# Kernel tuning notes

Hardware: AMD Instinct MI355X
Metric: run time of the kernel (lower is better)

The kernel has to match this reference:

```python
import jax, jax.numpy as jnp
import numpy as np
from jax import lax

EPS = 1e-12


def _conv_block(x, w, scale, bias, pool):
    # x: (N, Cin, H, W), w: (Cout, Cin, 3, 3). BN in eval mode folded into scale/bias.
    y = lax.conv_general_dilated(x, w, window_strides=(1, 1), padding='SAME',
                                 dimension_numbers=('NCHW', 'OIHW', 'NCHW'))
    y = y * scale[None, :, None, None] + bias[None, :, None, None]
    y = jax.nn.relu(y)
    if pool:
        y = lax.reduce_window(y, -jnp.inf, lax.max, (1, 1, 2, 2), (1, 1, 2, 2), 'VALID')
    return y


def _encoder(x, w1, s1, b1, w2, s2, b2, w3, s3, b3, w4, s4, b4):
    x = _conv_block(x, w1, s1, b1, True)
    x = _conv_block(x, w2, s2, b2, True)
    x = _conv_block(x, w3, s3, b3, False)
    x = _conv_block(x, w4, s4, b4, False)
    return x  # (N, 64, 21, 21)


def _l2norm(x, axis):
    n = jnp.sqrt(jnp.sum(x * x, axis=axis, keepdims=True))
    return x / jnp.maximum(n, EPS)


def setup_inputs() -> dict:
    key = jax.random.key(0)
    ks = jax.random.split(key, 8)
    B, NQ, Way, Shot, C, H, W = 2, 75, 5, 5, 3, 84, 84
    D = 64
    inp = {
        'query': jax.random.normal(ks[0], (B, NQ, C, H, W), jnp.float32),
        'support': jax.random.normal(ks[1], (B, Way, Shot, C, H, W), jnp.float32),
        'w1': jax.random.normal(ks[2], (D, C, 3, 3), jnp.float32) * 0.1,
        'w2': jax.random.normal(ks[3], (D, D, 3, 3), jnp.float32) * 0.05,
        'w3': jax.random.normal(ks[4], (D, D, 3, 3), jnp.float32) * 0.05,
        'w4': jax.random.normal(ks[5], (D, D, 3, 3), jnp.float32) * 0.05,
    }
    for i in range(1, 5):
        inp[f's{i}'] = jnp.ones((D,), jnp.float32)
        inp[f'b{i}'] = jnp.zeros((D,), jnp.float32)
    return inp


def reference(query, support, w1, s1, b1, w2, s2, b2, w3, s3, b3, w4, s4, b4):
    B, NQ, C, H, W = query.shape
    _, Way, Shot, _, _, _ = support.shape
    q_flat = query.reshape(B * NQ, C, H, W)
    s_flat = support.reshape(B * Way * Shot, C, H, W)
    q_feat = _encoder(q_flat, w1, s1, b1, w2, s2, b2, w3, s3, b3, w4, s4, b4)
    s_feat = _encoder(s_flat, w1, s1, b1, w2, s2, b2, w3, s3, b3, w4, s4, b4)
    D, h, w = q_feat.shape[1], q_feat.shape[2], q_feat.shape[3]
    HW = h * w
    q_local = _l2norm(q_feat.reshape(B, NQ, D, HW), axis=2)            # (B,NQ,D,HW)
    s_local = s_feat.reshape(B, Way, Shot, D, HW).mean(axis=2)          # mean over shots
    s_local = _l2norm(s_local, axis=2)                                  # (B,Way,D,HW)
    # all pairwise local cosine similarities, batched in one einsum
    sim = jnp.einsum('bqdm,bcdn->bqcmn', q_local, s_local)              # (B,NQ,Way,HW,HW)
    best = sim.max(axis=-1)                                             # best match per query descriptor
    scores = best.mean(axis=-1)                                         # (B,NQ,Way)
    return scores.reshape(B * NQ, Way)
```

## Files before the change

kernel.cpp:

```cpp
#include <hip/hip_runtime.h>

#define EPS 1e-12f

#define NIMG   200
#define NQIMG  150
#define BDIM   2
#define NQ     75
#define WAY    5
#define SHOT   5
#define DCH    64
#define H1     84
#define H2     42
#define H3     21
#define HW2    1764
#define HW3    441
#define PH     86
#define PSZ    7396
#define SST    448

typedef __attribute__((ext_vector_type(8))) short bf16x8;
typedef __attribute__((ext_vector_type(4))) float f32x4;

__device__ __forceinline__ unsigned short f2bf(float f) {
    unsigned u = __float_as_uint(f);
    u += 0x7fffu + ((u >> 16) & 1u);
    return (unsigned short)(u >> 16);
}
__device__ __forceinline__ float bf2f(unsigned short h) {
    return __uint_as_float(((unsigned)h) << 16);
}
__device__ __forceinline__ int swz(int pix, int c) {
    return pix * 128 + ((c ^ ((pix >> 1) & 7)) << 4);
}

__global__ __launch_bounds__(256) void pad_in(
    const float* __restrict__ qin, const float* __restrict__ sin_,
    unsigned short* __restrict__ pad)
{
    int idx = blockIdx.x * 256 + threadIdx.x;
    if (idx >= NIMG * 3 * PSZ) return;
    int img = idx / (3 * PSZ);
    int rem = idx % (3 * PSZ);
    int ci = rem / PSZ, p = rem % PSZ;
    int iy = p / PH, ix = p % PH;
    float v = 0.f;
    if (iy >= 1 && iy <= H1 && ix >= 1 && ix <= H1) {
        const float* src = (img < NQIMG) ? (qin + (size_t)img * 3 * H1 * H1)
                                         : (sin_ + (size_t)(img - NQIMG) * 3 * H1 * H1);
        v = src[(size_t)ci * H1 * H1 + (iy - 1) * H1 + (ix - 1)];
    }
    pad[idx] = f2bf(v);
}

__global__ __launch_bounds__(256) void pack_w1(
    const float* __restrict__ w1, const float* __restrict__ s1,
    unsigned short* __restrict__ p1)
{
    int idx = blockIdx.x * 256 + threadIdx.x;
    if (idx >= 2048) return;
    int j = idx & 7, lane = (idx >> 3) & 63, mt = idx >> 9;
    int co = (mt << 4) + (lane & 15);
    int k = ((lane >> 4) << 3) + j;
    float v = 0.f;
    if (k < 27) {
        int ci = k / 9, s = k % 9;
        v = w1[(co * 3 + ci) * 9 + s] * s1[co];
    }
    p1[idx] = f2bf(v);
}

__global__ __launch_bounds__(256) void pack_w(
    const float* __restrict__ w2, const float* __restrict__ s2,
    const float* __restrict__ w3, const float* __restrict__ s3,
    const float* __restrict__ w4, const float* __restrict__ s4,
    unsigned short* __restrict__ p2, unsigned short* __restrict__ p3,
    unsigned short* __restrict__ p4)
{
    int idx = blockIdx.x * 256 + threadIdx.x;
    if (idx >= 3 * 36864) return;
    int which = idx / 36864;
    int r = idx % 36864;
    int j = r & 7, lane = (r >> 3) & 63, mt = (r >> 9) & 3, t = (r >> 11) & 1, s = r >> 12;
    int co = (mt << 4) + (lane & 15);
    int ci = (t << 5) + ((lane >> 4) << 3) + j;
    const float* w = (which == 0) ? w2 : (which == 1) ? w3 : w4;
    const float* sc = (which == 0) ? s2 : (which == 1) ? s3 : s4;
    unsigned short* p = (which == 0) ? p2 : (which == 1) ? p3 : p4;
    p[r] = f2bf(w[(co * 64 + ci) * 9 + s] * sc[co]);
}

__global__ __launch_bounds__(256) void conv1_mfma(
    const unsigned short* __restrict__ pad,
    const unsigned short* __restrict__ wp1,
    const float* __restrict__ bias,
    unsigned short* __restrict__ out)
{
    int img = blockIdx.x / 7, seg = blockIdx.x % 7;
    int tid = threadIdx.x;
    __shared__ unsigned short strip[3 * 14 * 86];

    const unsigned* srcd = (const unsigned*)pad;
    size_t ibase = (size_t)img * 3 * (PSZ / 2);
    #pragma unroll
    for (int it = 0; it < 8; it++) {
        int i = it * 256 + tid;
        if (i < 1806) {
            int ci = i / 602, r = i % 602;
            ((unsigned*)strip)[i] = srcd[ibase + ci * (PSZ / 2) + 516 * seg + r];
        }
    }
    __syncthreads();

    int wv = tid >> 6, lane = tid & 63;
    int lc = lane & 15, kg = lane >> 4;

    const bf16x8* wvv = (const bf16x8*)wp1;
    bf16x8 a0 = wvv[lane];
    bf16x8 a1 = wvv[64 + lane];
    bf16x8 a2 = wvv[128 + lane];
    bf16x8 a3 = wvv[192 + lane];

    int off[8];
    #pragma unroll
    for (int j = 0; j < 8; j++) {
        int k = (kg << 3) + j;
        int kk = k < 27 ? k : 0;
        int ci = kk / 9, s = kk % 9;
        off[j] = ci * 1204 + (s / 3) * 86 + (s % 3);
    }

    f32x4 bini[4];
    #pragma unroll
    for (int mt = 0; mt < 4; mt++) {
        float4 bq = *reinterpret_cast<const float4*>(bias + (mt << 4) + (kg << 2));
        bini[mt] = (f32x4){bq.x, bq.y, bq.z, bq.w};
    }

    #pragma unroll
    for (int it = 0; it < 4; it++) {
        int pl = it * 64 + wv * 16 + lc;
        bool valid = pl < 252;
        int plc = valid ? pl : 251;
        int pyl = plc / 42, pxl = plc % 42;
        int base = pyl * 172 + 2 * pxl;

        bf16x8 b[4];
        #pragma unroll
        for (int j = 0; j < 8; j++) {
            int a = base + off[j];
            b[0][j] = (short)strip[a];
            b[1][j] = (short)strip[a + 1];
            b[2][j] = (short)strip[a + 86];
            b[3][j] = (short)strip[a + 87];
        }

        f32x4 acc[4][4];
        #pragma unroll
        for (int mt = 0; mt < 4; mt++)
            #pragma unroll
            for (int sub = 0; sub < 4; sub++)
                acc[mt][sub] = bini[mt];
        #pragma unroll
        for (int sub = 0; sub < 4; sub++) {
            acc[0][sub] = __builtin_amdgcn_mfma_f32_16x16x32_bf16(a0, b[sub], acc[0][sub], 0, 0, 0);
            acc[1][sub] = __builtin_amdgcn_mfma_f32_16x16x32_bf16(a1, b[sub], acc[1][sub], 0, 0, 0);
            acc[2][sub] = __builtin_amdgcn_mfma_f32_16x16x32_bf16(a2, b[sub], acc[2][sub], 0, 0, 0);
            acc[3][sub] = __builtin_amdgcn_mfma_f32_16x16x32_bf16(a3, b[sub], acc[3][sub], 0, 0, 0);
        }

        if (valid) {
            int p = seg * 252 + pl;
            #pragma unroll
            for (int mt = 0; mt < 4; mt++) {
                unsigned short uo[4];
                #pragma unroll
                for (int r = 0; r < 4; r++) {
                    float m = fmaxf(fmaxf(acc[mt][0][r], acc[mt][1][r]),
                                    fmaxf(acc[mt][2][r], acc[mt][3][r]));
                    uo[r] = f2bf(fmaxf(m, 0.f));
                }
                uint2 pk;
                pk.x = (unsigned)uo[0] | ((unsigned)uo[1] << 16);
                pk.y = (unsigned)uo[2] | ((unsigned)uo[3] << 16);
                *reinterpret_cast<uint2*>(out + ((size_t)img * HW2 + p) * DCH + (mt << 4) + (kg << 2)) = pk;
            }
        }
    }
}

__global__ __launch_bounds__(256) void conv2_mfma_pool(
    const unsigned short* __restrict__ act,
    const unsigned short* __restrict__ wp,
    const float* __restrict__ bias,
    unsigned short* __restrict__ out)
{
    int img = blockIdx.x / 7, tg = blockIdx.x % 7;
    int tid = threadIdx.x;
    __shared__ unsigned short lds[8 * 44 * DCH];

    const unsigned short* ab = act + (size_t)img * HW2 * DCH;
    int ybase = 6 * tg - 1;
    #pragma unroll
    for (int it = 0; it < 11; it++) {
        int idx = it * 256 + tid;
        int pix = idx >> 3, c = idx & 7;
        int r = pix / 44, xx = pix % 44;
        int y = ybase + r, x = xx - 1;
        bf16x8 v = (bf16x8)(short)0;
        if ((unsigned)y < (unsigned)H2 && (unsigned)x < (unsigned)H2)
            v = *(const bf16x8*)(ab + ((size_t)(y * H2 + x)) * DCH + (c << 3));
        *(bf16x8*)((char*)lds + swz(pix, c)) = v;
    }
    __syncthreads();

    int wv = tid >> 6, lane = tid & 63;
    int lc = lane & 15, kg = lane >> 4;
    int p_local = wv * 16 + lc;
    bool valid = p_local < 63;
    int pl = valid ? p_local : 62;
    int pyl = pl / 21, pxl = pl % 21;
    int pixc[4];
    #pragma unroll
    for (int sub = 0; sub < 4; sub++)
        pixc[sub] = (2 * pyl + (sub >> 1) + 1) * 44 + (2 * pxl + (sub & 1) + 1);

    f32x4 bini[4];
    #pragma unroll
    for (int mt = 0; mt < 4; mt++) {
        float4 bq = *reinterpret_cast<const float4*>(bias + (mt << 4) + (kg << 2));
        bini[mt] = (f32x4){bq.x, bq.y, bq.z, bq.w};
    }

    const bf16x8* wvv = (const bf16x8*)wp;
    f32x4 acc[4][4];
    #pragma unroll
    for (int i = 0; i < 4; i++)
        #pragma unroll
        for (int j = 0; j < 4; j++)
            acc[i][j] = bini[i];

    for (int s = 0; s < 9; s++) {
        int offs = (s / 3 - 1) * 44 + (s % 3 - 1);
        #pragma unroll
        for (int t = 0; t < 2; t++) {
            int fbase = ((s * 2 + t) * 4) << 6;
            bf16x8 a0 = wvv[fbase + lane];
            bf16x8 a1 = wvv[fbase + 64 + lane];
            bf16x8 a2 = wvv[fbase + 128 + lane];
            bf16x8 a3 = wvv[fbase + 192 + lane];
            int c = (t << 2) + kg;
            bf16x8 b[4];
            #pragma unroll
            for (int sub = 0; sub < 4; sub++) {
                int pix = pixc[sub] + offs;
                b[sub] = *(const bf16x8*)((const char*)lds + swz(pix, c));
            }
            #pragma unroll
            for (int sub = 0; sub < 4; sub++) {
                acc[0][sub] = __builtin_amdgcn_mfma_f32_16x16x32_bf16(a0, b[sub], acc[0][sub], 0, 0, 0);
                acc[1][sub] = __builtin_amdgcn_mfma_f32_16x16x32_bf16(a1, b[sub], acc[1][sub], 0, 0, 0);
                acc[2][sub] = __builtin_amdgcn_mfma_f32_16x16x32_bf16(a2, b[sub], acc[2][sub], 0, 0, 0);
                acc[3][sub] = __builtin_amdgcn_mfma_f32_16x16x32_bf16(a3, b[sub], acc[3][sub], 0, 0, 0);
            }
        }
    }

    if (!valid) return;
    int p = tg * 63 + p_local;
    #pragma unroll
    for (int mt = 0; mt < 4; mt++) {
        unsigned short uo[4];
        #pragma unroll
        for (int r = 0; r < 4; r++) {
            float m = fmaxf(fmaxf(acc[mt][0][r], acc[mt][1][r]),
                            fmaxf(acc[mt][2][r], acc[mt][3][r]));
            uo[r] = f2bf(fmaxf(m, 0.f));
        }
        uint2 pk;
        pk.x = (unsigned)uo[0] | ((unsigned)uo[1] << 16);
        pk.y = (unsigned)uo[2] | ((unsigned)uo[3] << 16);
        *reinterpret_cast<uint2*>(out + ((size_t)img * HW3 + p) * DCH + (mt << 4) + (kg << 2)) = pk;
    }
}

__global__ __launch_bounds__(256) void conv34_mfma(
    const unsigned short* __restrict__ act,
    const unsigned short* __restrict__ wp,
    const float* __restrict__ bias,
    unsigned short* __restrict__ out)
{
    int img = blockIdx.x;
    int tid = threadIdx.x;
    __shared__ unsigned short lds[529 * DCH];

    const unsigned short* ab = act + (size_t)img * HW3 * DCH;
    #pragma unroll
    for (int it = 0; it < 17; it++) {
        int idx = it * 256 + tid;
        if (idx < 529 * 8) {
            int pix = idx >> 3, c = idx & 7;
            int r = pix / 23, xx = pix % 23;
            int y = r - 1, x = xx - 1;
            bf16x8 v = (bf16x8)(short)0;
            if ((unsigned)y < (unsigned)H3 && (unsigned)x < (unsigned)H3)
                v = *(const bf16x8*)(ab + ((size_t)(y * H3 + x)) * DCH + (c << 3));
            *(bf16x8*)((char*)lds + swz(pix, c)) = v;
        }
    }
    __syncthreads();

    int wv = tid >> 6, lane = tid & 63;
    int lc = lane & 15, kg = lane >> 4;
    int pixBase[7];
    bool pv[7];
    #pragma unroll
    for (int i = 0; i < 7; i++) {
        int p = (wv * 7 + i) * 16 + lc;
        pv[i] = p < HW3;
        int pc = pv[i] ? p : HW3 - 1;
        pixBase[i] = (pc / 21) * 23 + (pc % 21);
    }

    f32x4 bini[4];
    #pragma unroll
    for (int mt = 0; mt < 4; mt++) {
        float4 bq = *reinterpret_cast<const float4*>(bias + (mt << 4) + (kg << 2));
        bini[mt] = (f32x4){bq.x, bq.y, bq.z, bq.w};
    }

    const bf16x8* wvv = (const bf16x8*)wp;
    f32x4 acc[7][4];
    #pragma unroll
    for (int i = 0; i < 7; i++)
        #pragma unroll
        for (int m = 0; m < 4; m++)
            acc[i][m] = bini[m];

    for (int s = 0; s < 9; s++) {
        int offs = (s / 3) * 23 + (s % 3);
        #pragma unroll
        for (int t = 0; t < 2; t++) {
            int fbase = ((s * 2 + t) * 4) << 6;
            bf16x8 a0 = wvv[fbase + lane];
            bf16x8 a1 = wvv[fbase + 64 + lane];
            bf16x8 a2 = wvv[fbase + 128 + lane];
            bf16x8 a3 = wvv[fbase + 192 + lane];
            int c = (t << 2) + kg;
            #pragma unroll
            for (int i = 0; i < 7; i++) {
                int pix = pixBase[i] + offs;
                bf16x8 bb = *(const bf16x8*)((const char*)lds + swz(pix, c));
                acc[i][0] = __builtin_amdgcn_mfma_f32_16x16x32_bf16(a0, bb, acc[i][0], 0, 0, 0);
                acc[i][1] = __builtin_amdgcn_mfma_f32_16x16x32_bf16(a1, bb, acc[i][1], 0, 0, 0);
                acc[i][2] = __builtin_amdgcn_mfma_f32_16x16x32_bf16(a2, bb, acc[i][2], 0, 0, 0);
                acc[i][3] = __builtin_amdgcn_mfma_f32_16x16x32_bf16(a3, bb, acc[i][3], 0, 0, 0);
            }
        }
    }

    #pragma unroll
    for (int mt = 0; mt < 4; mt++) {
        #pragma unroll
        for (int i = 0; i < 7; i++) {
            if (!pv[i]) continue;
            int p = (wv * 7 + i) * 16 + lc;
            unsigned short uo[4];
            #pragma unroll
            for (int r = 0; r < 4; r++)
                uo[r] = f2bf(fmaxf(acc[i][mt][r], 0.f));
            uint2 pk;
            pk.x = (unsigned)uo[0] | ((unsigned)uo[1] << 16);
            pk.y = (unsigned)uo[2] | ((unsigned)uo[3] << 16);
            *reinterpret_cast<uint2*>(out + ((size_t)img * HW3 + p) * DCH + (mt << 4) + (kg << 2)) = pk;
        }
    }
}

__global__ __launch_bounds__(256) void q_norm(
    const unsigned short* __restrict__ feat, unsigned short* __restrict__ q_local)
{
    int idx = blockIdx.x * 256 + threadIdx.x;
    if (idx >= NQIMG * HW3) return;
    const bf16x8* f = (const bf16x8*)(feat + (size_t)idx * DCH);
    float v[DCH];
    float ss = 0.f;
    #pragma unroll
    for (int g = 0; g < 8; g++) {
        bf16x8 x = f[g];
        #pragma unroll
        for (int j = 0; j < 8; j++) {
            float vv = bf2f((unsigned short)x[j]);
            v[g * 8 + j] = vv;
            ss = fmaf(vv, vv, ss);
        }
    }
    float inv = 1.f / fmaxf(sqrtf(ss), EPS);
    bf16x8* o = (bf16x8*)(q_local + (size_t)idx * DCH);
    #pragma unroll
    for (int g = 0; g < 8; g++) {
        bf16x8 pk;
        #pragma unroll
        for (int j = 0; j < 8; j++) pk[j] = (short)f2bf(v[g * 8 + j] * inv);
        o[g] = pk;
    }
}

__global__ __launch_bounds__(256) void s_mean_norm(
    const unsigned short* __restrict__ feat, unsigned short* __restrict__ s_local)
{
    int idx = blockIdx.x * 256 + threadIdx.x;
    if (idx >= BDIM * WAY * SST) return;
    int hw = idx % SST;
    int bc = idx / SST;
    bf16x8* o = (bf16x8*)(s_local + (size_t)idx * DCH);
    if (hw >= HW3) {
        #pragma unroll
        for (int g = 0; g < 8; g++) o[g] = (bf16x8)(short)0;
        return;
    }
    int img0 = NQIMG + bc * SHOT;
    float v[DCH];
    #pragma unroll
    for (int d = 0; d < DCH; d++) v[d] = 0.f;
    for (int sh = 0; sh < SHOT; sh++) {
        const bf16x8* f = (const bf16x8*)(feat + ((size_t)(img0 + sh) * HW3 + hw) * DCH);
        #pragma unroll
        for (int g = 0; g < 8; g++) {
            bf16x8 x = f[g];
            #pragma unroll
            for (int j = 0; j < 8; j++)
                v[g * 8 + j] += bf2f((unsigned short)x[j]);
        }
    }
    float ss = 0.f;
    #pragma unroll
    for (int d = 0; d < DCH; d++) {
        v[d] *= (1.f / SHOT);
        ss = fmaf(v[d], v[d], ss);
    }
    float inv = 1.f / fmaxf(sqrtf(ss), EPS);
    #pragma unroll
    for (int g = 0; g < 8; g++) {
        bf16x8 pk;
        #pragma unroll
        for (int j = 0; j < 8; j++) pk[j] = (short)f2bf(v[g * 8 + j] * inv);
        o[g] = pk;
    }
}

__global__ __launch_bounds__(256) void sim_mfma(
    const unsigned short* __restrict__ qloc,
    const unsigned short* __restrict__ sloc,
    float* __restrict__ out)
{
    int blk = blockIdx.x;
    int imgq = blk / WAY, way = blk % WAY;
    int b = imgq / NQ;
    const unsigned short* qp = qloc + (size_t)imgq * HW3 * DCH;
    const unsigned short* sp = sloc + (size_t)(b * WAY + way) * SST * DCH;

    int tid = threadIdx.x;
    int wv = tid >> 6, lane = tid & 63;
    int lc = lane & 15, kg = lane >> 4;
    int mt0 = wv * 7;

    bf16x8 qa0[7], qa1[7];
    #pragma unroll
    for (int i = 0; i < 7; i++) {
        const unsigned short* qrow = qp + (size_t)((mt0 + i) * 16 + lc) * DCH + (kg << 3);
        qa0[i] = *(const bf16x8*)(qrow);
        qa1[i] = *(const bf16x8*)(qrow + 32);
    }
    f32x4 rmax[7];
    #pragma unroll
    for (int i = 0; i < 7; i++)
        rmax[i] = (f32x4){-1e30f, -1e30f, -1e30f, -1e30f};

    const f32x4 z4 = (f32x4){0.f, 0.f, 0.f, 0.f};
    const unsigned short* sbase = sp + (size_t)lc * DCH + (kg << 3);

    for (int t = 0; t < 13; t++) {
        const unsigned short* r0 = sbase + (size_t)(2 * t) * 16 * DCH;
        const unsigned short* r1 = r0 + 16 * DCH;
        bf16x8 sA0 = *(const bf16x8*)(r0);
        bf16x8 sA1 = *(const bf16x8*)(r0 + 32);
        bf16x8 sB0 = *(const bf16x8*)(r1);
        bf16x8 sB1 = *(const bf16x8*)(r1 + 32);
        #pragma unroll
        for (int i = 0; i < 7; i++) {
            f32x4 aA = __builtin_amdgcn_mfma_f32_16x16x32_bf16(qa0[i], sA0, z4, 0, 0, 0);
            aA = __builtin_amdgcn_mfma_f32_16x16x32_bf16(qa1[i], sA1, aA, 0, 0, 0);
            f32x4 aB = __builtin_amdgcn_mfma_f32_16x16x32_bf16(qa0[i], sB0, z4, 0, 0, 0);
            aB = __builtin_amdgcn_mfma_f32_16x16x32_bf16(qa1[i], sB1, aB, 0, 0, 0);
            #pragma unroll
            for (int r = 0; r < 4; r++)
                rmax[i][r] = fmaxf(rmax[i][r], fmaxf(aA[r], aB[r]));
        }
    }
    {
        const unsigned short* r0 = sbase + (size_t)26 * 16 * DCH;
        const unsigned short* r1 = r0 + 16 * DCH;
        bf16x8 sA0 = *(const bf16x8*)(r0);
        bf16x8 sA1 = *(const bf16x8*)(r0 + 32);
        bf16x8 sB0 = *(const bf16x8*)(r1);
        bf16x8 sB1 = *(const bf16x8*)(r1 + 32);
        bool nval = (432 + lc) < HW3;
        #pragma unroll
        for (int i = 0; i < 7; i++) {
            f32x4 aA = __builtin_amdgcn_mfma_f32_16x16x32_bf16(qa0[i], sA0, z4, 0, 0, 0);
            aA = __builtin_amdgcn_mfma_f32_16x16x32_bf16(qa1[i], sA1, aA, 0, 0, 0);
            f32x4 aB = __builtin_amdgcn_mfma_f32_16x16x32_bf16(qa0[i], sB0, z4, 0, 0, 0);
            aB = __builtin_amdgcn_mfma_f32_16x16x32_bf16(qa1[i], sB1, aB, 0, 0, 0);
            #pragma unroll
            for (int r = 0; r < 4; r++)
                rmax[i][r] = fmaxf(rmax[i][r], fmaxf(aA[r], nval ? aB[r] : -1e30f));
        }
    }

    float msum = 0.f;
    #pragma unroll
    for (int i = 0; i < 7; i++) {
        #pragma unroll
        for (int r = 0; r < 4; r++) {
            float v = rmax[i][r];
            v = fmaxf(v, __shfl_xor(v, 1, 64));
            v = fmaxf(v, __shfl_xor(v, 2, 64));
            v = fmaxf(v, __shfl_xor(v, 4, 64));
            v = fmaxf(v, __shfl_xor(v, 8, 64));
            int m = (mt0 + i) * 16 + (kg << 2) + r;
            if (lc == 0 && m < HW3) msum += v;
        }
    }
    #pragma unroll
    for (int off = 32; off > 0; off >>= 1)
        msum += __shfl_xor(msum, off, 64);
    __shared__ float red[4];
    if (lane == 0) red[wv] = msum;
    __syncthreads();
    if (tid == 0)
        out[(size_t)imgq * WAY + way] = (red[0] + red[1] + red[2] + red[3]) * (1.f / HW3);
}

extern "C" void kernel_launch(void* const* d_in, const int* in_sizes, int n_in,
                              void* d_out, int out_size, void* d_ws, size_t ws_size,
                              hipStream_t stream) {
    const float* query   = (const float*)d_in[0];
    const float* support = (const float*)d_in[1];
    const float* w1 = (const float*)d_in[2];
    const float* w2 = (const float*)d_in[3];
    const float* w3 = (const float*)d_in[4];
    const float* w4 = (const float*)d_in[5];
    const float* s1 = (const float*)d_in[6];
    const float* b1 = (const float*)d_in[7];
    const float* s2 = (const float*)d_in[8];
    const float* b2 = (const float*)d_in[9];
    const float* s3 = (const float*)d_in[10];
    const float* b3 = (const float*)d_in[11];
    const float* s4 = (const float*)d_in[12];
    const float* b4 = (const float*)d_in[13];
    float* out = (float*)d_out;

    char* ws = (char*)d_ws;
    unsigned short* A1  = (unsigned short*)(ws);
    unsigned short* A2  = (unsigned short*)(ws + 45158400);
    unsigned short* A3  = (unsigned short*)(ws + 56448000);
    unsigned short* A4  = (unsigned short*)(ws + 67737600);
    unsigned short* QL  = (unsigned short*)(ws + 79027200);
    unsigned short* SL  = (unsigned short*)(ws + 87494400);
    unsigned short* WP2 = (unsigned short*)(ws + 88067840);
    unsigned short* WP3 = (unsigned short*)(ws + 88141568);
    unsigned short* WP4 = (unsigned short*)(ws + 88215296);
    unsigned short* WP1 = (unsigned short*)(ws + 88289024);
    unsigned short* PAD = (unsigned short*)(ws + 88293120);

    pad_in<<<(NIMG * 3 * PSZ + 255) / 256, 256, 0, stream>>>(query, support, PAD);
    pack_w1<<<8, 256, 0, stream>>>(w1, s1, WP1);
    pack_w<<<(3 * 36864 + 255) / 256, 256, 0, stream>>>(w2, s2, w3, s3, w4, s4, WP2, WP3, WP4);

    conv1_mfma<<<NIMG * 7, 256, 0, stream>>>(PAD, WP1, b1, A1);
    conv2_mfma_pool<<<NIMG * 7, 256, 0, stream>>>(A1, WP2, b2, A2);
    conv34_mfma<<<NIMG, 256, 0, stream>>>(A2, WP3, b3, A3);
    conv34_mfma<<<NIMG, 256, 0, stream>>>(A3, WP4, b4, A4);

    q_norm<<<(NQIMG * HW3 + 255) / 256, 256, 0, stream>>>(A4, QL);
    s_mean_norm<<<(BDIM * WAY * SST + 255) / 256, 256, 0, stream>>>(A4, SL);

    sim_mfma<<<NQIMG * WAY, 256, 0, stream>>>(QL, SL, out);
}
```

Before: 153.6 us.

## Fuse conv3, conv4 and query L2-norm into one kernel; merge prep kernels

Merges the padding and weight-packing kernels into a single launch. Conv3 and conv4 now run in one kernel: conv3 output is written back into the padded LDS tile, the halo is re-zeroed, and conv4 computes from LDS. For query images the epilogue applies the L2 normalisation in registers via cross-lane shuffles, so the A3 round trip, the separate q_norm pass and several launches are removed. The cost is that each block does twice the work on only 200 blocks, so fewer waves are in flight while the two convolutions run.

```diff
diff --git a/kernel.cpp b/kernel.cpp
--- a/kernel.cpp
+++ b/kernel.cpp
@@ -18,6 +18,10 @@
 #define PSZ    7396
 #define SST    448
 
+#define PAD_BLKS  17335
+#define W1_BLKS   8
+#define W_BLKS    432
+
 typedef __attribute__((ext_vector_type(8))) short bf16x8;
 typedef __attribute__((ext_vector_type(4))) float f32x4;
 
@@ -33,60 +37,54 @@
     return pix * 128 + ((c ^ ((pix >> 1) & 7)) << 4);
 }
 
-__global__ __launch_bounds__(256) void pad_in(
+__global__ __launch_bounds__(256) void prep(
     const float* __restrict__ qin, const float* __restrict__ sin_,
-    unsigned short* __restrict__ pad)
-{
-    int idx = blockIdx.x * 256 + threadIdx.x;
-    if (idx >= NIMG * 3 * PSZ) return;
-    int img = idx / (3 * PSZ);
-    int rem = idx % (3 * PSZ);
-    int ci = rem / PSZ, p = rem % PSZ;
-    int iy = p / PH, ix = p % PH;
-    float v = 0.f;
-    if (iy >= 1 && iy <= H1 && ix >= 1 && ix <= H1) {
-        const float* src = (img < NQIMG) ? (qin + (size_t)img * 3 * H1 * H1)
-                                         : (sin_ + (size_t)(img - NQIMG) * 3 * H1 * H1);
-        v = src[(size_t)ci * H1 * H1 + (iy - 1) * H1 + (ix - 1)];
-    }
-    pad[idx] = f2bf(v);
-}
-
-__global__ __launch_bounds__(256) void pack_w1(
     const float* __restrict__ w1, const float* __restrict__ s1,
-    unsigned short* __restrict__ p1)
-{
-    int idx = blockIdx.x * 256 + threadIdx.x;
-    if (idx >= 2048) return;
-    int j = idx & 7, lane = (idx >> 3) & 63, mt = idx >> 9;
-    int co = (mt << 4) + (lane & 15);
-    int k = ((lane >> 4) << 3) + j;
-    float v = 0.f;
-    if (k < 27) {
-        int ci = k / 9, s = k % 9;
-        v = w1[(co * 3 + ci) * 9 + s] * s1[co];
-    }
-    p1[idx] = f2bf(v);
-}
-
-__global__ __launch_bounds__(256) void pack_w(
     const float* __restrict__ w2, const float* __restrict__ s2,
     const float* __restrict__ w3, const float* __restrict__ s3,
     const float* __restrict__ w4, const float* __restrict__ s4,
+    unsigned short* __restrict__ pad, unsigned short* __restrict__ p1,
     unsigned short* __restrict__ p2, unsigned short* __restrict__ p3,
     unsigned short* __restrict__ p4)
 {
-    int idx = blockIdx.x * 256 + threadIdx.x;
-    if (idx >= 3 * 36864) return;
-    int which = idx / 36864;
-    int r = idx % 36864;
-    int j = r & 7, lane = (r >> 3) & 63, mt = (r >> 9) & 3, t = (r >> 11) & 1, s = r >> 12;
-    int co = (mt << 4) + (lane & 15);
-    int ci = (t << 5) + ((lane >> 4) << 3) + j;
-    const float* w = (which == 0) ? w2 : (which == 1) ? w3 : w4;
-    const float* sc = (which == 0) ? s2 : (which == 1) ? s3 : s4;
-    unsigned short* p = (which == 0) ? p2 : (which == 1) ? p3 : p4;
-    p[r] = f2bf(w[(co * 64 + ci) * 9 + s] * sc[co]);
+    int blk = blockIdx.x;
+    if (blk < PAD_BLKS) {
+        int idx = blk * 256 + threadIdx.x;
+        if (idx >= NIMG * 3 * PSZ) return;
+        int img = idx / (3 * PSZ);
+        int rem = idx % (3 * PSZ);
+        int ci = rem / PSZ, p = rem % PSZ;
+        int iy = p / PH, ix = p % PH;
+        float v = 0.f;
+        if (iy >= 1 && iy <= H1 && ix >= 1 && ix <= H1) {
+            const float* src = (img < NQIMG) ? (qin + (size_t)img * 3 * H1 * H1)
+                                             : (sin_ + (size_t)(img - NQIMG) * 3 * H1 * H1);
+            v = src[(size_t)ci * H1 * H1 + (iy - 1) * H1 + (ix - 1)];
+        }
+        pad[idx] = f2bf(v);
+    } else if (blk < PAD_BLKS + W1_BLKS) {
+        int idx = (blk - PAD_BLKS) * 256 + threadIdx.x;
+        int j = idx & 7, lane = (idx >> 3) & 63, mt = idx >> 9;
+        int co = (mt << 4) + (lane & 15);
+        int k = ((lane >> 4) << 3) + j;
+        float v = 0.f;
+        if (k < 27) {
+            int ci = k / 9, s = k % 9;
+            v = w1[(co * 3 + ci) * 9 + s] * s1[co];
+        }
+        p1[idx] = f2bf(v);
+    } else {
+        int idx = (blk - PAD_BLKS - W1_BLKS) * 256 + threadIdx.x;
+        int which = idx / 36864;
+        int r = idx % 36864;
+        int j = r & 7, lane = (r >> 3) & 63, mt = (r >> 9) & 3, t = (r >> 11) & 1, s = r >> 12;
+        int co = (mt << 4) + (lane & 15);
+        int ci = (t << 5) + ((lane >> 4) << 3) + j;
+        const float* w = (which == 0) ? w2 : (which == 1) ? w3 : w4;
+        const float* sc = (which == 0) ? s2 : (which == 1) ? s3 : s4;
+        unsigned short* p = (which == 0) ? p2 : (which == 1) ? p3 : p4;
+        p[r] = f2bf(w[(co * 64 + ci) * 9 + s] * sc[co]);
+    }
 }
 
 __global__ __launch_bounds__(256) void conv1_mfma(
@@ -283,11 +281,12 @@
     }
 }
 
-__global__ __launch_bounds__(256) void conv34_mfma(
+__global__ __launch_bounds__(256) void conv34_fused(
     const unsigned short* __restrict__ act,
-    const unsigned short* __restrict__ wp,
-    const float* __restrict__ bias,
-    unsigned short* __restrict__ out)
+    const unsigned short* __restrict__ wp3, const unsigned short* __restrict__ wp4,
+    const float* __restrict__ b3, const float* __restrict__ b4,
+    unsigned short* __restrict__ a4out,
+    unsigned short* __restrict__ qlout)
 {
     int img = blockIdx.x;
     int tid = threadIdx.x;
@@ -324,11 +323,10 @@
     f32x4 bini[4];
     #pragma unroll
     for (int mt = 0; mt < 4; mt++) {
-        float4 bq = *reinterpret_cast<const float4*>(bias + (mt << 4) + (kg << 2));
+        float4 bq = *reinterpret_cast<const float4*>(b3 + (mt << 4) + (kg << 2));
         bini[mt] = (f32x4){bq.x, bq.y, bq.z, bq.w};
     }
 
-    const bf16x8* wvv = (const bf16x8*)wp;
     f32x4 acc[7][4];
     #pragma unroll
     for (int i = 0; i < 7; i++)
@@ -336,15 +334,16 @@
         for (int m = 0; m < 4; m++)
             acc[i][m] = bini[m];
 
+    const bf16x8* wv3 = (const bf16x8*)wp3;
     for (int s = 0; s < 9; s++) {
         int offs = (s / 3) * 23 + (s % 3);
         #pragma unroll
         for (int t = 0; t < 2; t++) {
             int fbase = ((s * 2 + t) * 4) << 6;
-            bf16x8 a0 = wvv[fbase + lane];
-            bf16x8 a1 = wvv[fbase + 64 + lane];
-            bf16x8 a2 = wvv[fbase + 128 + lane];
-            bf16x8 a3 = wvv[fbase + 192 + lane];
+            bf16x8 a0 = wv3[fbase + lane];
+            bf16x8 a1 = wv3[fbase + 64 + lane];
+            bf16x8 a2 = wv3[fbase + 128 + lane];
+            bf16x8 a3 = wv3[fbase + 192 + lane];
             int c = (t << 2) + kg;
             #pragma unroll
             for (int i = 0; i < 7; i++) {
@@ -358,12 +357,14 @@
         }
     }
 
-    #pragma unroll
-    for (int mt = 0; mt < 4; mt++) {
-        #pragma unroll
-        for (int i = 0; i < 7; i++) {
-            if (!pv[i]) continue;
-            int p = (wv * 7 + i) * 16 + lc;
+    __syncthreads();
+
+    #pragma unroll
+    for (int i = 0; i < 7; i++) {
+        if (!pv[i]) continue;
+        int pix = pixBase[i] + 24;
+        #pragma unroll
+        for (int mt = 0; mt < 4; mt++) {
             unsigned short uo[4];
             #pragma unroll
             for (int r = 0; r < 4; r++)
@@ -371,37 +372,105 @@
             uint2 pk;
             pk.x = (unsigned)uo[0] | ((unsigned)uo[1] << 16);
             pk.y = (unsigned)uo[2] | ((unsigned)uo[3] << 16);
-            *reinterpret_cast<uint2*>(out + ((size_t)img * HW3 + p) * DCH + (mt << 4) + (kg << 2)) = pk;
-        }
-    }
-}
-
-__global__ __launch_bounds__(256) void q_norm(
-    const unsigned short* __restrict__ feat, unsigned short* __restrict__ q_local)
-{
-    int idx = blockIdx.x * 256 + threadIdx.x;
-    if (idx >= NQIMG * HW3) return;
-    const bf16x8* f = (const bf16x8*)(feat + (size_t)idx * DCH);
-    float v[DCH];
-    float ss = 0.f;
-    #pragma unroll
-    for (int g = 0; g < 8; g++) {
-        bf16x8 x = f[g];
-        #pragma unroll
-        for (int j = 0; j < 8; j++) {
-            float vv = bf2f((unsigned short)x[j]);
-            v[g * 8 + j] = vv;
-            ss = fmaf(vv, vv, ss);
-        }
-    }
-    float inv = 1.f / fmaxf(sqrtf(ss), EPS);
-    bf16x8* o = (bf16x8*)(q_local + (size_t)idx * DCH);
-    #pragma unroll
-    for (int g = 0; g < 8; g++) {
-        bf16x8 pk;
-        #pragma unroll
-        for (int j = 0; j < 8; j++) pk[j] = (short)f2bf(v[g * 8 + j] * inv);
-        o[g] = pk;
+            int c = (mt << 1) + (kg >> 1);
+            *(uint2*)((char*)lds + swz(pix, c) + ((kg & 1) << 3)) = pk;
+        }
+    }
+    #pragma unroll
+    for (int it = 0; it < 3; it++) {
+        int idx = it * 256 + tid;
+        if (idx < 704) {
+            int j = idx >> 3, c = idx & 7;
+            int pix;
+            if (j < 23)      pix = j;
+            else if (j < 46) pix = 506 + (j - 23);
+            else { int k = j - 46; pix = (1 + (k >> 1)) * 23 + (k & 1) * 22; }
+            *(bf16x8*)((char*)lds + swz(pix, c)) = (bf16x8)(short)0;
+        }
+    }
+    __syncthreads();
+
+    #pragma unroll
+    for (int mt = 0; mt < 4; mt++) {
+        float4 bq = *reinterpret_cast<const float4*>(b4 + (mt << 4) + (kg << 2));
+        bini[mt] = (f32x4){bq.x, bq.y, bq.z, bq.w};
+    }
+    #pragma unroll
+    for (int i = 0; i < 7; i++)
+        #pragma unroll
+        for (int m = 0; m < 4; m++)
+            acc[i][m] = bini[m];
+
+    const bf16x8* wv4 = (const bf16x8*)wp4;
+    for (int s = 0; s < 9; s++) {
+        int offs = (s / 3) * 23 + (s % 3);
+        #pragma unroll
+        for (int t = 0; t < 2; t++) {
+            int fbase = ((s * 2 + t) * 4) << 6;
+            bf16x8 a0 = wv4[fbase + lane];
+            bf16x8 a1 = wv4[fbase + 64 + lane];
+            bf16x8 a2 = wv4[fbase + 128 + lane];
+            bf16x8 a3 = wv4[fbase + 192 + lane];
+            int c = (t << 2) + kg;
+            #pragma unroll
+            for (int i = 0; i < 7; i++) {
+                int pix = pixBase[i] + offs;
+                bf16x8 bb = *(const bf16x8*)((const char*)lds + swz(pix, c));
+                acc[i][0] = __builtin_amdgcn_mfma_f32_16x16x32_bf16(a0, bb, acc[i][0], 0, 0, 0);
+                acc[i][1] = __builtin_amdgcn_mfma_f32_16x16x32_bf16(a1, bb, acc[i][1], 0, 0, 0);
+                acc[i][2] = __builtin_amdgcn_mfma_f32_16x16x32_bf16(a2, bb, acc[i][2], 0, 0, 0);
+                acc[i][3] = __builtin_amdgcn_mfma_f32_16x16x32_bf16(a3, bb, acc[i][3], 0, 0, 0);
+            }
+        }
+    }
+
+    if (img < NQIMG) {
+        #pragma unroll
+        for (int i = 0; i < 7; i++) {
+            float v[4][4];
+            float ssq = 0.f;
+            #pragma unroll
+            for (int mt = 0; mt < 4; mt++)
+                #pragma unroll
+                for (int r = 0; r < 4; r++) {
+                    float x = fmaxf(acc[i][mt][r], 0.f);
+                    v[mt][r] = x;
+                    ssq = fmaf(x, x, ssq);
+                }
+            ssq += __shfl_xor(ssq, 16, 64);
+            ssq += __shfl_xor(ssq, 32, 64);
+            float inv = 1.f / fmaxf(sqrtf(ssq), EPS);
+            if (!pv[i]) continue;
+            int p = (wv * 7 + i) * 16 + lc;
+            #pragma unroll
+            for (int mt = 0; mt < 4; mt++) {
+                unsigned short uo[4];
+                #pragma unroll
+                for (int r = 0; r < 4; r++)
+                    uo[r] = f2bf(v[mt][r] * inv);
+                uint2 pk;
+                pk.x = (unsigned)uo[0] | ((unsigned)uo[1] << 16);
+                pk.y = (unsigned)uo[2] | ((unsigned)uo[3] << 16);
+                *reinterpret_cast<uint2*>(qlout + ((size_t)img * HW3 + p) * DCH + (mt << 4) + (kg << 2)) = pk;
+            }
+        }
+    } else {
+        #pragma unroll
+        for (int mt = 0; mt < 4; mt++) {
+            #pragma unroll
+            for (int i = 0; i < 7; i++) {
+                if (!pv[i]) continue;
+                int p = (wv * 7 + i) * 16 + lc;
+                unsigned short uo[4];
+                #pragma unroll
+                for (int r = 0; r < 4; r++)
+                    uo[r] = f2bf(fmaxf(acc[i][mt][r], 0.f));
+                uint2 pk;
+                pk.x = (unsigned)uo[0] | ((unsigned)uo[1] << 16);
+                pk.y = (unsigned)uo[2] | ((unsigned)uo[3] << 16);
+                *reinterpret_cast<uint2*>(a4out + ((size_t)img * HW3 + p) * DCH + (mt << 4) + (kg << 2)) = pk;
+            }
+        }
     }
 }
 
@@ -563,26 +632,22 @@
     char* ws = (char*)d_ws;
     unsigned short* A1  = (unsigned short*)(ws);
     unsigned short* A2  = (unsigned short*)(ws + 45158400);
-    unsigned short* A3  = (unsigned short*)(ws + 56448000);
-    unsigned short* A4  = (unsigned short*)(ws + 67737600);
-    unsigned short* QL  = (unsigned short*)(ws + 79027200);
-    unsigned short* SL  = (unsigned short*)(ws + 87494400);
-    unsigned short* WP2 = (unsigned short*)(ws + 88067840);
-    unsigned short* WP3 = (unsigned short*)(ws + 88141568);
-    unsigned short* WP4 = (unsigned short*)(ws + 88215296);
-    unsigned short* WP1 = (unsigned short*)(ws + 88289024);
-    unsigned short* PAD = (unsigned short*)(ws + 88293120);
-
-    pad_in<<<(NIMG * 3 * PSZ + 255) / 256, 256, 0, stream>>>(query, support, PAD);
-    pack_w1<<<8, 256, 0, stream>>>(w1, s1, WP1);
-    pack_w<<<(3 * 36864 + 255) / 256, 256, 0, stream>>>(w2, s2, w3, s3, w4, s4, WP2, WP3, WP4);
+    unsigned short* A4  = (unsigned short*)(ws + 56448000);
+    unsigned short* QL  = (unsigned short*)(ws + 67737600);
+    unsigned short* SL  = (unsigned short*)(ws + 76204800);
+    unsigned short* WP2 = (unsigned short*)(ws + 76778240);
+    unsigned short* WP3 = (unsigned short*)(ws + 76851968);
+    unsigned short* WP4 = (unsigned short*)(ws + 76925696);
+    unsigned short* WP1 = (unsigned short*)(ws + 76999424);
+    unsigned short* PAD = (unsigned short*)(ws + 77003520);
+
+    prep<<<PAD_BLKS + W1_BLKS + W_BLKS, 256, 0, stream>>>(
+        query, support, w1, s1, w2, s2, w3, s3, w4, s4, PAD, WP1, WP2, WP3, WP4);
 
     conv1_mfma<<<NIMG * 7, 256, 0, stream>>>(PAD, WP1, b1, A1);
     conv2_mfma_pool<<<NIMG * 7, 256, 0, stream>>>(A1, WP2, b2, A2);
-    conv34_mfma<<<NIMG, 256, 0, stream>>>(A2, WP3, b3, A3);
-    conv34_mfma<<<NIMG, 256, 0, stream>>>(A3, WP4, b4, A4);
-
-    q_norm<<<(NQIMG * HW3 + 255) / 256, 256, 0, stream>>>(A4, QL);
+    conv34_fused<<<NIMG, 256, 0, stream>>>(A2, WP3, WP4, b3, b4, A4, QL);
+
     s_mean_norm<<<(BDIM * WAY * SST + 255) / 256, 256, 0, stream>>>(A4, SL);
 
     sim_mfma<<<NQIMG * WAY, 256, 0, stream>>>(QL, SL, out);
```

New measurement: 136.7 us. 11.0% less time.
